# Kernel optimization log

Measured on AMD Instinct MI355X. Metric: run time of the kernel, lower is better.

## Reference

```python
import jax, jax.numpy as jnp
import numpy as np

N = 4096      # num_nodes
B = 32        # batch
U = 64        # num_units
L = 2         # num_rnn_layers
K = 2         # max_diffusion_step
OUT = 1       # output_dim (also decoder input_dim)
NM = 2 * K + 1  # num_matrices: 2 supports * K cheb steps + identity


def _random_walk_T(adj):
    # calculate_random_walk_matrix(adj).T : (D^-1 W)^T
    d = adj.sum(axis=1)
    return (adj / d[:, None]).T


def setup_inputs():
    key = jax.random.key(0)
    ks = jax.random.split(key, 16)
    adj = jax.random.uniform(ks[0], (N, N), dtype=jnp.float32)
    S_fwd = _random_walk_T(adj)      # forward transition, transposed
    S_bwd = _random_walk_T(adj.T)    # backward transition, transposed

    inputs = jax.random.normal(ks[1], (B, N, OUT), dtype=jnp.float32)
    hidden_state = jax.random.normal(ks[2], (L, B, N, U), dtype=jnp.float32) * 0.1

    D0 = OUT + U   # layer 0 gconv input width
    D1 = U + U     # layer 1 gconv input width
    s = 0.05
    Wg0 = jax.random.normal(ks[3], (NM * D0, 2 * U), jnp.float32) * s
    bg0 = jnp.ones((2 * U,), jnp.float32)          # bias_start = 1.0 for gates
    Wc0 = jax.random.normal(ks[4], (NM * D0, U), jnp.float32) * s
    bc0 = jnp.zeros((U,), jnp.float32)
    Wg1 = jax.random.normal(ks[5], (NM * D1, 2 * U), jnp.float32) * s
    bg1 = jnp.ones((2 * U,), jnp.float32)
    Wc1 = jax.random.normal(ks[6], (NM * D1, U), jnp.float32) * s
    bc1 = jnp.zeros((U,), jnp.float32)
    Wp = jax.random.normal(ks[7], (U, OUT), jnp.float32) * s
    bp = jnp.zeros((OUT,), jnp.float32)
    return {
        "inputs": inputs, "hidden_state": hidden_state,
        "S_fwd": S_fwd, "S_bwd": S_bwd,
        "Wg0": Wg0, "bg0": bg0, "Wc0": Wc0, "bc0": bc0,
        "Wg1": Wg1, "bg1": bg1, "Wc1": Wc1, "bc1": bc1,
        "Wp": Wp, "bp": bp,
    }


def _gconv(supports, x, h, W, b):
    # diffusion graph convolution with Chebyshev recursion (DCRNN)
    x0 = jnp.concatenate([x, h], axis=-1)      # (B, N, D)
    xs = [x0]
    for S in supports:
        x1 = jnp.einsum('mn,bnd->bmd', S, x0)
        xs.append(x1)
        xk_2, xk_1 = x0, x1
        for _ in range(K - 1):
            x2 = 2.0 * jnp.einsum('mn,bnd->bmd', S, xk_1) - xk_2
            xs.append(x2)
            xk_2, xk_1 = xk_1, x2
    X = jnp.concatenate(xs, axis=-1)           # (B, N, NM*D)
    return X @ W + b


def _dcgru_cell(supports, x, h, Wg, bg, Wc, bc):
    value = jax.nn.sigmoid(_gconv(supports, x, h, Wg, bg))   # (B, N, 2U)
    r, u = jnp.split(value, 2, axis=-1)
    c = jnp.tanh(_gconv(supports, x, r * h, Wc, bc))
    return u * h + (1.0 - u) * c


def reference(inputs, hidden_state, S_fwd, S_bwd,
              Wg0, bg0, Wc0, bc0, Wg1, bg1, Wc1, bc1, Wp, bp):
    supports = (S_fwd, S_bwd)
    layer_params = [(Wg0, bg0, Wc0, bc0), (Wg1, bg1, Wc1, bc1)]
    out = inputs
    new_hidden = []
    for i, (Wg, bg, Wc, bc) in enumerate(layer_params):
        h = _dcgru_cell(supports, out, hidden_state[i], Wg, bg, Wc, bc)
        new_hidden.append(h)
        out = h
    predict = out @ Wp + bp                    # (B, N, OUT)
    return predict, jnp.stack(new_hidden)
```

## Files before the change

### kernel.cpp

```cpp
#include <hip/hip_runtime.h>

typedef unsigned short u16;
typedef unsigned int u32;
typedef unsigned long long u64;
typedef short v8s __attribute__((ext_vector_type(8)));
typedef float v4f __attribute__((ext_vector_type(4)));

#define NN 4096
#define BATCH 32

__device__ __forceinline__ float b2f(u16 u) {
  union { u32 i; float f; } c; c.i = ((u32)u) << 16; return c.f;
}
__device__ __forceinline__ u16 f2b(float f) {
  union { float f; u32 i; } c; c.f = f;
  u32 x = c.i;
  return (u16)((x + 0x7fffu + ((x >> 16) & 1u)) >> 16);
}
__device__ __forceinline__ u32 pk2(float a, float b) {
  return (u32)f2b(a) | ((u32)f2b(b) << 16);
}

typedef const __attribute__((address_space(1))) u32* gp_t;
typedef __attribute__((address_space(3))) u32* lp_t;
__device__ __forceinline__ void gld16(const u16* g, u16* l) {
  __builtin_amdgcn_global_load_lds((gp_t)g, (lp_t)l, 16, 0, 0);
}

#define CBAR() asm volatile("" ::: "memory")
#define BARRIER() do { CBAR(); __builtin_amdgcn_s_barrier(); CBAR(); } while (0)
#define LGKM0() asm volatile("s_waitcnt lgkmcnt(0)" ::: "memory")
#define VMC4() asm volatile("s_waitcnt vmcnt(4)" ::: "memory")
#define VMC3() asm volatile("s_waitcnt vmcnt(3)" ::: "memory")
#define VMC0() asm volatile("s_waitcnt vmcnt(0)" ::: "memory")

__global__ __launch_bounds__(256) void cvtS(const float* __restrict__ S,
                                            u16* __restrict__ Sb) {
  const u64 idx = ((u64)blockIdx.x * 256 + threadIdx.x) * 8;
  const float4 a = *(const float4*)(S + idx);
  const float4 b = *(const float4*)(S + idx + 4);
  uint4 o;
  o.x = pk2(a.x, a.y); o.y = pk2(a.z, a.w);
  o.z = pk2(b.x, b.y); o.w = pk2(b.z, b.w);
  *(uint4*)(Sb + idx) = o;
}

__global__ __launch_bounds__(512, 2) void gemm256(const u16* __restrict__ A,
                                                  const u16* __restrict__ B,
                                                  u16* __restrict__ Ct,
                                                  const u16* __restrict__ Xt) {
  __shared__ __align__(16) u16 lds[65536];
  const int t = threadIdx.x;
  const int wave = t >> 6, lane = t & 63;
  const int q = lane >> 4, r16 = lane & 15;
  const int wm = wave >> 2, wn = wave & 3;

  const int nwg = (int)(gridDim.x * gridDim.y);
  const int bid = (int)(blockIdx.y * gridDim.x + blockIdx.x);
  const int swz = (bid & 7) * (nwg >> 3) + (bid >> 3);
  const int m0 = (swz & 15) << 8;
  const int c0 = (swz >> 4) << 8;

  v4f acc[8][4];
  const v4f vz = {0.f, 0.f, 0.f, 0.f};
#pragma unroll
  for (int i = 0; i < 8; ++i)
#pragma unroll
    for (int j = 0; j < 4; ++j) acc[i][j] = vz;

  const int srow = t >> 3;
  const int sslot = ((t & 7) ^ (srow & 7)) << 3;
  const u16* pA = A + (u64)(m0 + srow) * NN + sslot;
  const u16* pB = B + (u64)(c0 + srow) * NN + sslot;
  const u64 rstep = (u64)64 * NN;
  const u64 hstep = (u64)128 * NN;
  u16* lw = lds + (wave << 9);

  const int sw8 = (q ^ (r16 & 7)) << 3;
  const int aBase = (wm << 13) + (r16 << 6) + sw8;
  const int bBase = 16384 + ((wn >> 1) << 13) + ((wn & 1) << 12) + (r16 << 6) + sw8;

  const int NT = NN >> 6;

  gld16(pA, lw);
  gld16(pA + rstep, lw + 4096);
  gld16(pA + hstep, lw + 8192);
  gld16(pA + hstep + rstep, lw + 12288);
  gld16(pB, lw + 16384);
  gld16(pB + rstep, lw + 20480);
  gld16(pB + hstep, lw + 24576);
  gld16(pB + hstep + rstep, lw + 28672);
  gld16(pB + 64, lw + 32768 + 16384);
  gld16(pB + 64 + rstep, lw + 32768 + 20480);
  gld16(pB + 64 + hstep, lw + 32768 + 24576);
  gld16(pB + 64 + hstep + rstep, lw + 32768 + 28672);
  VMC4();
  BARRIER();

  v8s af[4][2], bf01[2][2], bf23[2][2];
#pragma unroll
  for (int i = 0; i < 4; ++i) {
    const int a = aBase + (i << 10);
    af[i][0] = *(const v8s*)(lds + a);
    af[i][1] = *(const v8s*)(lds + (a ^ 32));
  }
#pragma unroll
  for (int j = 0; j < 2; ++j) {
    const int b = bBase + (j << 10);
    bf01[j][0] = *(const v8s*)(lds + b);
    bf01[j][1] = *(const v8s*)(lds + (b ^ 32));
  }

#pragma unroll 2
  for (int T = 0; T < NT; ++T) {
    const int bo = (T & 1) << 15;
    const int no = bo ^ 32768;
    const u64 ka = (u64)(T + 1 < NT ? T + 1 : NT - 1) << 6;
    const u64 kb = (u64)(T + 2 < NT ? T + 2 : NT - 1) << 6;

    gld16(pA + ka, lw + no);
    gld16(pA + ka + rstep, lw + no + 4096);
#pragma unroll
    for (int j = 0; j < 2; ++j) {
      const int b = bo + bBase + ((2 + j) << 10);
      bf23[j][0] = *(const v8s*)(lds + b);
      bf23[j][1] = *(const v8s*)(lds + (b ^ 32));
    }
    __builtin_amdgcn_s_setprio(1);
#pragma unroll
    for (int i = 0; i < 4; ++i)
#pragma unroll
      for (int j = 0; j < 2; ++j) {
        acc[i][j] = __builtin_amdgcn_mfma_f32_16x16x32_bf16(af[i][0], bf01[j][0], acc[i][j], 0, 0, 0);
        acc[i][j] = __builtin_amdgcn_mfma_f32_16x16x32_bf16(af[i][1], bf01[j][1], acc[i][j], 0, 0, 0);
      }
    __builtin_amdgcn_s_setprio(0);

    gld16(pA + hstep + ka, lw + no + 8192);
    gld16(pA + hstep + ka + rstep, lw + no + 12288);
    LGKM0();
    BARRIER();
    __builtin_amdgcn_s_setprio(1);
#pragma unroll
    for (int i = 0; i < 4; ++i)
#pragma unroll
      for (int j = 0; j < 2; ++j) {
        acc[i][2 + j] = __builtin_amdgcn_mfma_f32_16x16x32_bf16(af[i][0], bf23[j][0], acc[i][2 + j], 0, 0, 0);
        acc[i][2 + j] = __builtin_amdgcn_mfma_f32_16x16x32_bf16(af[i][1], bf23[j][1], acc[i][2 + j], 0, 0, 0);
      }
    __builtin_amdgcn_s_setprio(0);
#pragma unroll
    for (int i = 0; i < 4; ++i) {
      const int a = bo + aBase + ((4 + i) << 10);
      af[i][0] = *(const v8s*)(lds + a);
      af[i][1] = *(const v8s*)(lds + (a ^ 32));
    }
    __builtin_amdgcn_sched_barrier(0);

    gld16(pB + kb, lw + bo + 16384);
    gld16(pB + kb + rstep, lw + bo + 20480);
    __builtin_amdgcn_s_setprio(1);
#pragma unroll
    for (int i = 0; i < 4; ++i)
#pragma unroll
      for (int j = 0; j < 2; ++j) {
        acc[4 + i][2 + j] = __builtin_amdgcn_mfma_f32_16x16x32_bf16(af[i][0], bf23[j][0], acc[4 + i][2 + j], 0, 0, 0);
        acc[4 + i][2 + j] = __builtin_amdgcn_mfma_f32_16x16x32_bf16(af[i][1], bf23[j][1], acc[4 + i][2 + j], 0, 0, 0);
      }
    __builtin_amdgcn_s_setprio(0);

    gld16(pB + hstep + kb, lw + bo + 24576);
    gld16(pB + hstep + kb + rstep, lw + bo + 28672);
    VMC4();
    BARRIER();
    __builtin_amdgcn_s_setprio(1);
#pragma unroll
    for (int i = 0; i < 4; ++i)
#pragma unroll
      for (int j = 0; j < 2; ++j) {
        acc[4 + i][j] = __builtin_amdgcn_mfma_f32_16x16x32_bf16(af[i][0], bf01[j][0], acc[4 + i][j], 0, 0, 0);
        acc[4 + i][j] = __builtin_amdgcn_mfma_f32_16x16x32_bf16(af[i][1], bf01[j][1], acc[4 + i][j], 0, 0, 0);
      }
    __builtin_amdgcn_s_setprio(0);
#pragma unroll
    for (int i = 0; i < 4; ++i) {
      const int a = no + aBase + (i << 10);
      af[i][0] = *(const v8s*)(lds + a);
      af[i][1] = *(const v8s*)(lds + (a ^ 32));
    }
#pragma unroll
    for (int j = 0; j < 2; ++j) {
      const int b = no + bBase + (j << 10);
      bf01[j][0] = *(const v8s*)(lds + b);
      bf01[j][1] = *(const v8s*)(lds + (b ^ 32));
    }
    __builtin_amdgcn_sched_barrier(0);
  }

  VMC0();
  __syncthreads();
#pragma unroll
  for (int i = 0; i < 8; ++i)
#pragma unroll
    for (int j = 0; j < 4; ++j) {
      const int cl = (wn << 6) + (j << 4) + r16;
      const int ml = (wm << 7) + (i << 4) + (q << 2);
      const int phys = (cl << 8) + ((((ml >> 3) ^ (cl & 7)) << 3) | (ml & 7));
      uint2 pv;
      pv.x = pk2(acc[i][j][0], acc[i][j][1]);
      pv.y = pk2(acc[i][j][2], acc[i][j][3]);
      *(uint2*)(lds + phys) = pv;
    }
  __syncthreads();
#pragma unroll
  for (int it = 0; it < 16; ++it) {
    const int f = (it << 9) + t;
    const int cl = f >> 5, sl = f & 31;
    const int phys = (cl << 8) + ((sl ^ (cl & 7)) << 3);
    union { uint4 v; u16 e[8]; } tv;
    tv.v = *(const uint4*)(lds + phys);
    const u64 gi = (u64)(c0 + cl) * NN + m0 + (sl << 3);
    if (Xt) {
      union { uint4 v; u16 e[8]; } xv, ov;
      xv.v = *(const uint4*)(Xt + gi);
#pragma unroll
      for (int s = 0; s < 8; ++s) ov.e[s] = f2b(2.f * b2f(tv.e[s]) - b2f(xv.e[s]));
      *(uint4*)(Ct + gi) = ov.v;
    } else {
      *(uint4*)(Ct + gi) = tv.v;
    }
  }
}

__global__ __launch_bounds__(512, 2) void gemm192(const u16* __restrict__ A,
                                                  const u16* __restrict__ B,
                                                  u16* __restrict__ Ct,
                                                  const u16* __restrict__ Xt) {
  __shared__ __align__(16) u16 lds[57344];
  const int t = threadIdx.x;
  const int wave = t >> 6, lane = t & 63;
  const int q = lane >> 4, r16 = lane & 15;
  const int wm = wave >> 2, wn = wave & 3;

  const int nwg = (int)(gridDim.x * gridDim.y);
  const int bid = (int)(blockIdx.y * gridDim.x + blockIdx.x);
  const int swz = (bid & 7) * (nwg >> 3) + (bid >> 3);
  const int m0 = (swz & 15) << 8;
  const int c0 = (swz >> 4) * 192;

  v4f acc[8][3];
  const v4f vz = {0.f, 0.f, 0.f, 0.f};
#pragma unroll
  for (int i = 0; i < 8; ++i)
#pragma unroll
    for (int j = 0; j < 3; ++j) acc[i][j] = vz;

  const int srow = t >> 3;
  const int sslot = ((t & 7) ^ (srow & 7)) << 3;
  const u16* pA = A + (u64)(m0 + srow) * NN + sslot;
  const u16* pB = B + (u64)(c0 + srow) * NN + sslot;
  const u64 rstep = (u64)64 * NN;
  u16* lw = lds + (wave << 9);

  const int sw8 = (q ^ (r16 & 7)) << 3;
  const int aBase = (wm << 13) + (r16 << 6) + sw8;
  const int bBase = 16384 + wn * 3072 + (r16 << 6) + sw8;

  const int NT = NN >> 6;

  gld16(pA, lw);
  gld16(pA + rstep, lw + 4096);
  gld16(pA + 2 * rstep, lw + 8192);
  gld16(pA + 3 * rstep, lw + 12288);
  gld16(pB, lw + 16384);
  gld16(pB + rstep, lw + 20480);
  gld16(pB + 2 * rstep, lw + 24576);
  gld16(pB + 64, lw + 28672 + 16384);
  gld16(pB + 64 + rstep, lw + 28672 + 20480);
  gld16(pB + 64 + 2 * rstep, lw + 28672 + 24576);
  VMC3();
  BARRIER();

  v8s af[4][2], bf01[2][2], bf2[2];
#pragma unroll
  for (int i = 0; i < 4; ++i) {
    const int a = aBase + (i << 10);
    af[i][0] = *(const v8s*)(lds + a);
    af[i][1] = *(const v8s*)(lds + (a ^ 32));
  }
#pragma unroll
  for (int j = 0; j < 2; ++j) {
    const int b = bBase + (j << 10);
    bf01[j][0] = *(const v8s*)(lds + b);
    bf01[j][1] = *(const v8s*)(lds + (b ^ 32));
  }

#pragma unroll 2
  for (int T = 0; T < NT; ++T) {
    const int bo = (T & 1) ? 28672 : 0;
    const int no = bo ^ 28672;
    const u64 ka = (u64)(T + 1 < NT ? T + 1 : NT - 1) << 6;
    const u64 kb = (u64)(T + 2 < NT ? T + 2 : NT - 1) << 6;

    gld16(pA + ka, lw + no);
    gld16(pA + ka + rstep, lw + no + 4096);
    {
      const int b = bo + bBase + 2048;
      bf2[0] = *(const v8s*)(lds + b);
      bf2[1] = *(const v8s*)(lds + (b ^ 32));
    }
    __builtin_amdgcn_s_setprio(1);
#pragma unroll
    for (int i = 0; i < 4; ++i)
#pragma unroll
      for (int j = 0; j < 2; ++j) {
        acc[i][j] = __builtin_amdgcn_mfma_f32_16x16x32_bf16(af[i][0], bf01[j][0], acc[i][j], 0, 0, 0);
        acc[i][j] = __builtin_amdgcn_mfma_f32_16x16x32_bf16(af[i][1], bf01[j][1], acc[i][j], 0, 0, 0);
      }
    __builtin_amdgcn_s_setprio(0);

    gld16(pA + ka + 2 * rstep, lw + no + 8192);
    gld16(pA + ka + 3 * rstep, lw + no + 12288);
    LGKM0();
    BARRIER();
    __builtin_amdgcn_s_setprio(1);
#pragma unroll
    for (int i = 0; i < 4; ++i) {
      acc[i][2] = __builtin_amdgcn_mfma_f32_16x16x32_bf16(af[i][0], bf2[0], acc[i][2], 0, 0, 0);
      acc[i][2] = __builtin_amdgcn_mfma_f32_16x16x32_bf16(af[i][1], bf2[1], acc[i][2], 0, 0, 0);
    }
    __builtin_amdgcn_s_setprio(0);
#pragma unroll
    for (int i = 0; i < 4; ++i) {
      const int a = bo + aBase + ((4 + i) << 10);
      af[i][0] = *(const v8s*)(lds + a);
      af[i][1] = *(const v8s*)(lds + (a ^ 32));
    }
    __builtin_amdgcn_sched_barrier(0);

    gld16(pB + kb, lw + bo + 16384);
    gld16(pB + kb + rstep, lw + bo + 20480);
    __builtin_amdgcn_s_setprio(1);
#pragma unroll
    for (int i = 0; i < 4; ++i) {
      acc[4 + i][2] = __builtin_amdgcn_mfma_f32_16x16x32_bf16(af[i][0], bf2[0], acc[4 + i][2], 0, 0, 0);
      acc[4 + i][2] = __builtin_amdgcn_mfma_f32_16x16x32_bf16(af[i][1], bf2[1], acc[4 + i][2], 0, 0, 0);
    }
    __builtin_amdgcn_s_setprio(0);

    gld16(pB + kb + 2 * rstep, lw + bo + 24576);
    __builtin_amdgcn_s_setprio(1);
#pragma unroll
    for (int i = 0; i < 4; ++i)
#pragma unroll
      for (int j = 0; j < 2; ++j) {
        acc[4 + i][j] = __builtin_amdgcn_mfma_f32_16x16x32_bf16(af[i][0], bf01[j][0], acc[4 + i][j], 0, 0, 0);
        acc[4 + i][j] = __builtin_amdgcn_mfma_f32_16x16x32_bf16(af[i][1], bf01[j][1], acc[4 + i][j], 0, 0, 0);
      }
    __builtin_amdgcn_s_setprio(0);
    VMC3();
    BARRIER();
#pragma unroll
    for (int i = 0; i < 4; ++i) {
      const int a = no + aBase + (i << 10);
      af[i][0] = *(const v8s*)(lds + a);
      af[i][1] = *(const v8s*)(lds + (a ^ 32));
    }
#pragma unroll
    for (int j = 0; j < 2; ++j) {
      const int b = no + bBase + (j << 10);
      bf01[j][0] = *(const v8s*)(lds + b);
      bf01[j][1] = *(const v8s*)(lds + (b ^ 32));
    }
    __builtin_amdgcn_sched_barrier(0);
  }

  VMC0();
  __syncthreads();
#pragma unroll
  for (int i = 0; i < 8; ++i)
#pragma unroll
    for (int j = 0; j < 3; ++j) {
      const int cl = wn * 48 + j * 16 + r16;
      const int ml = (wm << 7) + (i << 4) + (q << 2);
      const int phys = (cl << 8) + ((((ml >> 3) ^ (cl & 7)) << 3) | (ml & 7));
      uint2 pv;
      pv.x = pk2(acc[i][j][0], acc[i][j][1]);
      pv.y = pk2(acc[i][j][2], acc[i][j][3]);
      *(uint2*)(lds + phys) = pv;
    }
  __syncthreads();
#pragma unroll
  for (int it = 0; it < 12; ++it) {
    const int f = (it << 9) + t;
    const int cl = f >> 5, sl = f & 31;
    const int phys = (cl << 8) + ((sl ^ (cl & 7)) << 3);
    union { uint4 v; u16 e[8]; } tv;
    tv.v = *(const uint4*)(lds + phys);
    const u64 gi = (u64)(c0 + cl) * NN + m0 + (sl << 3);
    if (Xt) {
      union { uint4 v; u16 e[8]; } xv, ov;
      xv.v = *(const uint4*)(Xt + gi);
#pragma unroll
      for (int s = 0; s < 8; ++s) ov.e[s] = f2b(2.f * b2f(tv.e[s]) - b2f(xv.e[s]));
      *(uint4*)(Ct + gi) = ov.v;
    } else {
      *(uint4*)(Ct + gi) = tv.v;
    }
  }
}

__global__ __launch_bounds__(256) void gemm_s(const float* __restrict__ A,
                                              const u16* __restrict__ B,
                                              u16* __restrict__ Ct,
                                              const u16* __restrict__ Xt) {
  __shared__ __align__(16) u16 As[4096];
  __shared__ __align__(16) u16 Bs[4096];
  __shared__ __align__(16) u16 T[16384];
  const int t = threadIdx.x;
  const int wave = t >> 6, lane = t & 63;
  const int m0 = blockIdx.x << 7, c0 = blockIdx.y << 7;
  const int wm = (wave >> 1) << 6, wc = (wave & 1) << 6;
  const int q = lane >> 4, r16 = lane & 15;
  v4f acc[4][4];
  const v4f vz = {0.f, 0.f, 0.f, 0.f};
#pragma unroll
  for (int i = 0; i < 4; ++i)
#pragma unroll
    for (int j = 0; j < 4; ++j) acc[i][j] = vz;

  const int sr = t >> 2;
  const int sc = (t & 3) << 3;
  const u64 abase = (u64)(m0 + sr) * NN + sc;
  const u64 bbase = (u64)(c0 + sr) * NN + sc;
  const u64 rstep = (u64)64 * NN;
  u16* as0 = As + sr * 32 + sc;
  u16* as1 = As + (64 + sr) * 32 + sc;
  u16* bs0 = Bs + sr * 32 + sc;
  u16* bs1 = Bs + (64 + sr) * 32 + sc;

  for (int k0 = 0; k0 < NN; k0 += 32) {
    const float4 a0l = *(const float4*)(A + abase + k0);
    const float4 a0h = *(const float4*)(A + abase + k0 + 4);
    const float4 a1l = *(const float4*)(A + abase + rstep + k0);
    const float4 a1h = *(const float4*)(A + abase + rstep + k0 + 4);
    const uint4 b0 = *(const uint4*)(B + bbase + k0);
    const uint4 b1 = *(const uint4*)(B + bbase + rstep + k0);
    uint4 pa0, pa1;
    pa0.x = pk2(a0l.x, a0l.y); pa0.y = pk2(a0l.z, a0l.w);
    pa0.z = pk2(a0h.x, a0h.y); pa0.w = pk2(a0h.z, a0h.w);
    pa1.x = pk2(a1l.x, a1l.y); pa1.y = pk2(a1l.z, a1l.w);
    pa1.z = pk2(a1h.x, a1h.y); pa1.w = pk2(a1h.z, a1h.w);
    __syncthreads();
    *(uint4*)as0 = pa0;
    *(uint4*)as1 = pa1;
    *(uint4*)bs0 = b0;
    *(uint4*)bs1 = b1;
    __syncthreads();
    v8s af[4], bf[4];
#pragma unroll
    for (int i = 0; i < 4; ++i)
      af[i] = *(const v8s*)(As + ((wm + i * 16 + r16) << 5) + (q << 3));
#pragma unroll
    for (int j = 0; j < 4; ++j)
      bf[j] = *(const v8s*)(Bs + ((wc + j * 16 + r16) << 5) + (q << 3));
#pragma unroll
    for (int i = 0; i < 4; ++i)
#pragma unroll
      for (int j = 0; j < 4; ++j)
        acc[i][j] = __builtin_amdgcn_mfma_f32_16x16x32_bf16(af[i], bf[j], acc[i][j], 0, 0, 0);
  }
#pragma unroll
  for (int i = 0; i < 4; ++i)
#pragma unroll
    for (int j = 0; j < 4; ++j) {
      const int cl = wc + j * 16 + r16;
      const int mm = wm + i * 16 + (q << 2);
      uint2 pv;
      pv.x = pk2(acc[i][j][0], acc[i][j][1]);
      pv.y = pk2(acc[i][j][2], acc[i][j][3]);
      *(uint2*)(T + (cl << 7) + mm) = pv;
    }
  __syncthreads();
#pragma unroll
  for (int it = 0; it < 8; ++it) {
    const int flat = it * 256 + t;
    const int cl = flat >> 4;
    const int seg = (flat & 15) << 3;
    const u64 gi = (u64)(c0 + cl) * NN + m0 + seg;
    union { uint4 v; u16 e[8]; } tv;
    tv.v = *(uint4*)(T + (cl << 7) + seg);
    if (Xt) {
      union { uint4 v; u16 e[8]; } xv, ov;
      xv.v = *(const uint4*)(Xt + gi);
#pragma unroll
      for (int s = 0; s < 8; ++s) ov.e[s] = f2b(2.f * b2f(tv.e[s]) - b2f(xv.e[s]));
      *(uint4*)(Ct + gi) = ov.v;
    } else {
      *(uint4*)(Ct + gi) = tv.v;
    }
  }
}

template <int DP, int KTOT>
__global__ __launch_bounds__(256) void proj_k(const u16* __restrict__ Wt,
                                              const u16* __restrict__ F,
                                              const float* __restrict__ bias,
                                              u16* __restrict__ outp,
                                              const int JSTR, const int ACT) {
  __shared__ __align__(16) u16 As2[2048];
  __shared__ __align__(16) u16 Bs2[4096];
  const int t = threadIdx.x;
  const int wave = t >> 6, lane = t & 63;
  const int q = lane >> 4, r16 = lane & 15;
  const int n0 = blockIdx.x << 7;
  const int j0 = blockIdx.y << 6;
  const int b = blockIdx.z;
  v4f acc[4][2];
  const v4f vz = {0.f, 0.f, 0.f, 0.f};
#pragma unroll
  for (int i = 0; i < 4; ++i) { acc[i][0] = vz; acc[i][1] = vz; }

  const int ar = t >> 2, ac = (t & 3) << 3;
  const u64 wbase = (u64)(j0 + ar) * KTOT + ac;

  for (int k0 = 0; k0 < KTOT; k0 += 32) {
    const uint4 av = *(const uint4*)(Wt + wbase + k0);
    uint4 bv[2];
#pragma unroll
    for (int ci = 0; ci < 2; ++ci) {
      const int c = ci * 256 + t;
      const int kr = c >> 4;
      const int seg = (c & 15) << 3;
      const int kk = k0 + kr;
      const int i = kk / DP;
      const int d = kk - i * DP;
      bv[ci] = *(const uint4*)(F + ((u64)i * (BATCH * DP) + (u64)b * DP + d) * NN + n0 + seg);
    }
    __syncthreads();
    *(uint4*)(As2 + ar * 32 + ac) = av;
#pragma unroll
    for (int ci = 0; ci < 2; ++ci) {
      const int c = ci * 256 + t;
      const int kr = c >> 4;
      const int seg = (c & 15) << 3;
      *(uint4*)(Bs2 + (kr << 7) + seg) = bv[ci];
    }
    __syncthreads();
    v8s af[4], bf[2];
#pragma unroll
    for (int i = 0; i < 4; ++i)
      af[i] = *(const v8s*)(As2 + ((i * 16 + r16) << 5) + (q << 3));
#pragma unroll
    for (int jj = 0; jj < 2; ++jj) {
      const int nn = (wave << 5) + jj * 16 + r16;
      v8s v;
#pragma unroll
      for (int s = 0; s < 8; ++s) v[s] = (short)Bs2[(((q << 3) + s) << 7) + nn];
      bf[jj] = v;
    }
#pragma unroll
    for (int i = 0; i < 4; ++i)
#pragma unroll
      for (int jj = 0; jj < 2; ++jj)
        acc[i][jj] = __builtin_amdgcn_mfma_f32_16x16x32_bf16(af[i], bf[jj], acc[i][jj], 0, 0, 0);
  }
#pragma unroll
  for (int i = 0; i < 4; ++i)
#pragma unroll
    for (int jj = 0; jj < 2; ++jj)
#pragma unroll
      for (int r = 0; r < 4; ++r) {
        const int j = j0 + i * 16 + (q << 2) + r;
        const int n = n0 + (wave << 5) + jj * 16 + r16;
        float v = acc[i][jj][r] + bias[j];
        v = ACT ? (1.f - 2.f / (__expf(2.f * v) + 1.f)) : (1.f / (1.f + __expf(-v)));
        outp[((u64)b * JSTR + j) * NN + n] = f2b(v);
      }
}

__global__ __launch_bounds__(256) void repackW(const float* __restrict__ W, u16* __restrict__ Wt,
                                               const int D, const int DP, const int KTOT,
                                               const int J) {
  const int idx = blockIdx.x * 256 + threadIdx.x;
  if (idx >= J * KTOT) return;
  const int j = idx / KTOT, k = idx - j * KTOT;
  const int i = k / DP, d = k - i * DP;
  u16 v = 0;
  if (i < 5 && d < D) v = f2b(W[(i * D + d) * J + j]);
  Wt[idx] = v;
}

__global__ __launch_bounds__(256) void pack0(const float* __restrict__ x,
                                             const float* __restrict__ hid0,
                                             u16* __restrict__ F0) {
  __shared__ __align__(16) u16 Hs[64 * 72];
  const int b = blockIdx.y, n0 = blockIdx.x << 6, t = threadIdx.x;
  const int r = t >> 2, ds = t & 3;
  const float* hrow = hid0 + ((u64)b * NN + n0 + r) * 64;
#pragma unroll
  for (int c4 = 0; c4 < 4; ++c4) {
    const float4 v = *(const float4*)(hrow + ds * 16 + c4 * 4);
    uint2 p;
    p.x = pk2(v.x, v.y);
    p.y = pk2(v.z, v.w);
    *(uint2*)(Hs + r * 72 + ds * 16 + c4 * 4) = p;
  }
  __syncthreads();
#pragma unroll
  for (int c2 = 0; c2 < 2; ++c2) {
    union { uint4 v; u16 h[8]; } o;
#pragma unroll
    for (int s = 0; s < 8; ++s) o.h[s] = Hs[(ds * 16 + c2 * 8 + s) * 72 + r];
    *(uint4*)(F0 + ((u64)b * 72 + 1 + r) * NN + n0 + ds * 16 + c2 * 8) = o.v;
  }
  if (t < 64) {
    F0[(u64)b * 72 * NN + n0 + t] = f2b(x[(u64)b * NN + n0 + t]);
  } else if (t < 120) {
    const int tt = t - 64;
    const int row = 65 + (tt >> 3), seg = (tt & 7) << 3;
    uint4 z; z.x = z.y = z.z = z.w = 0;
    *(uint4*)(F0 + ((u64)b * 72 + row) * NN + n0 + seg) = z;
  }
}

__global__ __launch_bounds__(256) void pack1(const float* __restrict__ hid1,
                                             u16* __restrict__ F1) {
  __shared__ __align__(16) u16 Hs[64 * 72];
  const int b = blockIdx.y, n0 = blockIdx.x << 6, t = threadIdx.x;
  const int r = t >> 2, ds = t & 3;
  const float* hrow = hid1 + ((u64)b * NN + n0 + r) * 64;
#pragma unroll
  for (int c4 = 0; c4 < 4; ++c4) {
    const float4 v = *(const float4*)(hrow + ds * 16 + c4 * 4);
    uint2 p;
    p.x = pk2(v.x, v.y);
    p.y = pk2(v.z, v.w);
    *(uint2*)(Hs + r * 72 + ds * 16 + c4 * 4) = p;
  }
  __syncthreads();
#pragma unroll
  for (int c2 = 0; c2 < 2; ++c2) {
    union { uint4 v; u16 h[8]; } o;
#pragma unroll
    for (int s = 0; s < 8; ++s) o.h[s] = Hs[(ds * 16 + c2 * 8 + s) * 72 + r];
    *(uint4*)(F1 + ((u64)b * 128 + 64 + r) * NN + n0 + ds * 16 + c2 * 8) = o.v;
  }
}

__global__ __launch_bounds__(256) void candpack(const u16* __restrict__ G, u16* __restrict__ F,
                                                const int DP, const int OFF) {
  const int u = blockIdx.x * 256 + threadIdx.x;
  const int b = u >> 15;
  const int d = (u >> 9) & 63;
  const int seg = (u & 511) << 3;
  union { uint4 v; u16 h[8]; } g, f, o;
  g.v = *(const uint4*)(G + ((u64)b * 128 + d) * NN + seg);
  u16* fp = F + ((u64)b * DP + OFF + d) * NN + seg;
  f.v = *(const uint4*)fp;
#pragma unroll
  for (int s = 0; s < 8; ++s) o.h[s] = f2b(b2f(f.h[s]) * b2f(g.h[s]));
  *(uint4*)fp = o.v;
}

__global__ __launch_bounds__(256) void hnew_k(const u16* __restrict__ G,
                                              const float* __restrict__ hidL,
                                              u16* __restrict__ HnF,
                                              float* __restrict__ outH) {
  __shared__ __align__(16) float Hs[64 * 72];
  __shared__ __align__(16) float T2[64 * 72];
  const int b = blockIdx.y, n0 = blockIdx.x << 6, t = threadIdx.x;
  const int r = t >> 2, ds = t & 3;
  const float* hrow = hidL + ((u64)b * NN + n0 + r) * 64;
#pragma unroll
  for (int c4 = 0; c4 < 4; ++c4)
    *(float4*)(Hs + r * 72 + ds * 16 + c4 * 4) = *(const float4*)(hrow + ds * 16 + c4 * 4);
  __syncthreads();
#pragma unroll
  for (int c2 = 0; c2 < 2; ++c2) {
    const int ncol = ds * 16 + c2 * 8;
    union { uint4 v; u16 h[8]; } uv, cv, o;
    uv.v = *(const uint4*)(G + ((u64)b * 128 + 64 + r) * NN + n0 + ncol);
    cv.v = *(const uint4*)(G + ((u64)b * 128 + r) * NN + n0 + ncol);
#pragma unroll
    for (int s = 0; s < 8; ++s) {
      const int nl = ncol + s;
      const float uu = b2f(uv.h[s]);
      const float hh = Hs[nl * 72 + r];
      const float cc = b2f(cv.h[s]);
      const float v = uu * hh + (1.f - uu) * cc;
      o.h[s] = f2b(v);
      T2[nl * 72 + r] = v;
    }
    *(uint4*)(HnF + ((u64)b * 128 + r) * NN + n0 + ncol) = o.v;
  }
  __syncthreads();
  const int nl2 = t >> 2, dseg = (t & 3) << 4;
#pragma unroll
  for (int c4 = 0; c4 < 4; ++c4) {
    const float4 v = *(const float4*)(T2 + nl2 * 72 + dseg + c4 * 4);
    *(float4*)(outH + ((u64)b * NN + n0 + nl2) * 64 + dseg + c4 * 4) = v;
  }
}

__global__ __launch_bounds__(256) void predictk(const float* __restrict__ H1bnd,
                                                const float* __restrict__ Wp,
                                                const float* __restrict__ bp,
                                                float* __restrict__ outp) {
  __shared__ float w[64];
  __shared__ float bb;
  const int t = threadIdx.x;
  if (t < 64) w[t] = Wp[t];
  if (t == 64) bb = bp[0];
  __syncthreads();
  const int idx = blockIdx.x * 256 + t;
  const float* h = H1bnd + (u64)idx * 64;
  float acc = bb;
#pragma unroll
  for (int c4 = 0; c4 < 16; ++c4) {
    const float4 v = *(const float4*)(h + c4 * 4);
    acc += v.x * w[c4 * 4] + v.y * w[c4 * 4 + 1] + v.z * w[c4 * 4 + 2] + v.w * w[c4 * 4 + 3];
  }
  outp[idx] = acc;
}

extern "C" void kernel_launch(void* const* d_in, const int* in_sizes, int n_in,
                              void* d_out, int out_size, void* d_ws, size_t ws_size,
                              hipStream_t stream) {
  const float* X   = (const float*)d_in[0];
  const float* HID = (const float*)d_in[1];
  const float* Sf  = (const float*)d_in[2];
  const float* Sb  = (const float*)d_in[3];
  const float* Wg0 = (const float*)d_in[4];
  const float* bg0 = (const float*)d_in[5];
  const float* Wc0 = (const float*)d_in[6];
  const float* bc0 = (const float*)d_in[7];
  const float* Wg1 = (const float*)d_in[8];
  const float* bg1 = (const float*)d_in[9];
  const float* Wc1 = (const float*)d_in[10];
  const float* bc1 = (const float*)d_in[11];
  const float* Wp  = (const float*)d_in[12];
  const float* bp  = (const float*)d_in[13];
  float* OUT = (float*)d_out;
  char* ws = (char*)d_ws;

  u16* F = (u16*)(ws);
  u16* G = (u16*)(ws + 167772160ull);
  const u64 NEED_BIG = 167772160ull + 33554432ull + 2ull * 33554432ull + 393216ull;
  const bool big = ws_size >= NEED_BIG;
  u16* Sfb = (u16*)(ws + 167772160ull + 33554432ull);
  u16* Sbb = Sfb + (u64)NN * NN;
  u16* WT = big ? (Sbb + (u64)NN * NN)
                : (u16*)(ws + 167772160ull + 33554432ull);
  u16* Wg0t = WT;
  u16* Wc0t = Wg0t + 128 * 384;
  u16* Wg1t = Wc0t + 64 * 384;
  u16* Wc1t = Wg1t + 128 * 640;

  const float* HID1 = HID + (u64)32 * 4096 * 64;
  float* OUT_H0 = OUT + 131072;
  float* OUT_H1 = OUT + 131072 + 8388608;

  hipMemsetAsync(ws + (u64)11520 * NN * 2, 0, (u64)2304 * NN * 2, stream);

  if (big) {
    cvtS<<<8192, 256, 0, stream>>>(Sf, Sfb);
    cvtS<<<8192, 256, 0, stream>>>(Sb, Sbb);
  }

  repackW<<<(128 * 384 + 255) / 256, 256, 0, stream>>>(Wg0, Wg0t, 65, 72, 384, 128);
  repackW<<<(64 * 384 + 255) / 256, 256, 0, stream>>>(Wc0, Wc0t, 65, 72, 384, 64);
  repackW<<<(128 * 640 + 255) / 256, 256, 0, stream>>>(Wg1, Wg1t, 128, 128, 640, 128);
  repackW<<<(64 * 640 + 255) / 256, 256, 0, stream>>>(Wc1, Wc1t, 128, 128, 640, 64);

  pack0<<<dim3(64, 32), 256, 0, stream>>>(X, HID, F);
  const u64 R0 = (u64)2304 * NN;
  const dim3 g192(16, 12);
  if (big) {
    gemm192<<<g192, 512, 0, stream>>>(Sfb, F, F + R0, nullptr);
    gemm192<<<g192, 512, 0, stream>>>(Sbb, F, F + 3 * R0, nullptr);
    gemm192<<<g192, 512, 0, stream>>>(Sfb, F + R0, F + 2 * R0, F);
    gemm192<<<g192, 512, 0, stream>>>(Sbb, F + 3 * R0, F + 4 * R0, F);
  } else {
    gemm_s<<<dim3(32, 18), 256, 0, stream>>>(Sf, F, F + R0, nullptr);
    gemm_s<<<dim3(32, 18), 256, 0, stream>>>(Sb, F, F + 3 * R0, nullptr);
    gemm_s<<<dim3(32, 18), 256, 0, stream>>>(Sf, F + R0, F + 2 * R0, F);
    gemm_s<<<dim3(32, 18), 256, 0, stream>>>(Sb, F + 3 * R0, F + 4 * R0, F);
  }
  proj_k<72, 384><<<dim3(32, 2, 32), 256, 0, stream>>>(Wg0t, F, bg0, G, 128, 0);
  candpack<<<4096, 256, 0, stream>>>(G, F, 72, 1);
  if (big) {
    gemm192<<<g192, 512, 0, stream>>>(Sfb, F, F + R0, nullptr);
    gemm192<<<g192, 512, 0, stream>>>(Sbb, F, F + 3 * R0, nullptr);
    gemm192<<<g192, 512, 0, stream>>>(Sfb, F + R0, F + 2 * R0, F);
    gemm192<<<g192, 512, 0, stream>>>(Sbb, F + 3 * R0, F + 4 * R0, F);
  } else {
    gemm_s<<<dim3(32, 18), 256, 0, stream>>>(Sf, F, F + R0, nullptr);
    gemm_s<<<dim3(32, 18), 256, 0, stream>>>(Sb, F, F + 3 * R0, nullptr);
    gemm_s<<<dim3(32, 18), 256, 0, stream>>>(Sf, F + R0, F + 2 * R0, F);
    gemm_s<<<dim3(32, 18), 256, 0, stream>>>(Sb, F + 3 * R0, F + 4 * R0, F);
  }
  proj_k<72, 384><<<dim3(32, 1, 32), 256, 0, stream>>>(Wc0t, F, bc0, G, 128, 1);
  hnew_k<<<dim3(64, 32), 256, 0, stream>>>(G, HID, F, OUT_H0);

  pack1<<<dim3(64, 32), 256, 0, stream>>>(HID1, F);
  const u64 R1 = (u64)4096 * NN;
  const dim3 g256(16, 16);
  if (big) {
    gemm256<<<g256, 512, 0, stream>>>(Sfb, F, F + R1, nullptr);
    gemm256<<<g256, 512, 0, stream>>>(Sbb, F, F + 3 * R1, nullptr);
    gemm256<<<g256, 512, 0, stream>>>(Sfb, F + R1, F + 2 * R1, F);
    gemm256<<<g256, 512, 0, stream>>>(Sbb, F + 3 * R1, F + 4 * R1, F);
  } else {
    gemm_s<<<dim3(32, 32), 256, 0, stream>>>(Sf, F, F + R1, nullptr);
    gemm_s<<<dim3(32, 32), 256, 0, stream>>>(Sb, F, F + 3 * R1, nullptr);
    gemm_s<<<dim3(32, 32), 256, 0, stream>>>(Sf, F + R1, F + 2 * R1, F);
    gemm_s<<<dim3(32, 32), 256, 0, stream>>>(Sb, F + 3 * R1, F + 4 * R1, F);
  }
  proj_k<128, 640><<<dim3(32, 2, 32), 256, 0, stream>>>(Wg1t, F, bg1, G, 128, 0);
  candpack<<<4096, 256, 0, stream>>>(G, F, 128, 64);
  if (big) {
    gemm256<<<g256, 512, 0, stream>>>(Sfb, F, F + R1, nullptr);
    gemm256<<<g256, 512, 0, stream>>>(Sbb, F, F + 3 * R1, nullptr);
    gemm256<<<g256, 512, 0, stream>>>(Sfb, F + R1, F + 2 * R1, F);
    gemm256<<<g256, 512, 0, stream>>>(Sbb, F + 3 * R1, F + 4 * R1, F);
  } else {
    gemm_s<<<dim3(32, 32), 256, 0, stream>>>(Sf, F, F + R1, nullptr);
    gemm_s<<<dim3(32, 32), 256, 0, stream>>>(Sb, F, F + 3 * R1, nullptr);
    gemm_s<<<dim3(32, 32), 256, 0, stream>>>(Sf, F + R1, F + 2 * R1, F);
    gemm_s<<<dim3(32, 32), 256, 0, stream>>>(Sb, F + 3 * R1, F + 4 * R1, F);
  }
  proj_k<128, 640><<<dim3(32, 1, 32), 256, 0, stream>>>(Wc1t, F, bc1, G, 128, 1);
  hnew_k<<<dim3(64, 32), 256, 0, stream>>>(G, HID1, F, OUT_H1);

  predictk<<<512, 256, 0, stream>>>(OUT_H1, Wp, bp, OUT);
}
```

Before: 1.875 ms.

## Retile layer-0 diffusion GEMM to 144 columns and fuse elementwise epilogues

The layer-0 support GEMM now uses a 256x144 tile with all eight waves split along M (2x9 accumulators per wave) instead of 256x192 with a 2x4 wave grid. The grid becomes 16x16 to cover the 2304 columns, which spreads the work over more workgroups. Separately, the r*h candidate packing is fused into the gate projection epilogue, and the output projection is fused into the final hnew kernel, removing two launches and a pass over memory. The risks are lower per-wave reuse in the narrower GEMM and a read-modify-write of F inside proj_k.

```diff
diff --git a/kernel.cpp b/kernel.cpp
--- a/kernel.cpp
+++ b/kernel.cpp
@@ -170,7 +170,7 @@
     __builtin_amdgcn_s_setprio(0);
 
     gld16(pB + hstep + kb, lw + bo + 24576);
-    gld16(pB + hstep + kb + rstep, lw + bo + 28672);
+    gld16(pB + hstep + rstep + kb, lw + bo + 28672);
     VMC4();
     BARRIER();
     __builtin_amdgcn_s_setprio(1);
@@ -232,7 +232,7 @@
   }
 }
 
-__global__ __launch_bounds__(512, 2) void gemm192(const u16* __restrict__ A,
+__global__ __launch_bounds__(512, 2) void gemm144(const u16* __restrict__ A,
                                                   const u16* __restrict__ B,
                                                   u16* __restrict__ Ct,
                                                   const u16* __restrict__ Xt) {
@@ -240,20 +240,20 @@
   const int t = threadIdx.x;
   const int wave = t >> 6, lane = t & 63;
   const int q = lane >> 4, r16 = lane & 15;
-  const int wm = wave >> 2, wn = wave & 3;
+  const int wm = wave;
 
   const int nwg = (int)(gridDim.x * gridDim.y);
   const int bid = (int)(blockIdx.y * gridDim.x + blockIdx.x);
   const int swz = (bid & 7) * (nwg >> 3) + (bid >> 3);
   const int m0 = (swz & 15) << 8;
-  const int c0 = (swz >> 4) * 192;
-
-  v4f acc[8][3];
+  const int c0 = (swz >> 4) * 144;
+
+  v4f acc[2][9];
   const v4f vz = {0.f, 0.f, 0.f, 0.f};
 #pragma unroll
-  for (int i = 0; i < 8; ++i)
-#pragma unroll
-    for (int j = 0; j < 3; ++j) acc[i][j] = vz;
+  for (int i = 0; i < 2; ++i)
+#pragma unroll
+    for (int j = 0; j < 9; ++j) acc[i][j] = vz;
 
   const int srow = t >> 3;
   const int sslot = ((t & 7) ^ (srow & 7)) << 3;
@@ -263,8 +263,8 @@
   u16* lw = lds + (wave << 9);
 
   const int sw8 = (q ^ (r16 & 7)) << 3;
-  const int aBase = (wm << 13) + (r16 << 6) + sw8;
-  const int bBase = 16384 + wn * 3072 + (r16 << 6) + sw8;
+  const int aBase = (wm << 11) + (r16 << 6) + sw8;
+  const int bBase = 16384 + (r16 << 6) + sw8;
 
   const int NT = NN >> 6;
 
@@ -281,18 +281,18 @@
   VMC3();
   BARRIER();
 
-  v8s af[4][2], bf01[2][2], bf2[2];
-#pragma unroll
-  for (int i = 0; i < 4; ++i) {
+  v8s af[2][2], bfA[5][2], bfB[4][2];
+#pragma unroll
+  for (int i = 0; i < 2; ++i) {
     const int a = aBase + (i << 10);
     af[i][0] = *(const v8s*)(lds + a);
     af[i][1] = *(const v8s*)(lds + (a ^ 32));
   }
 #pragma unroll
-  for (int j = 0; j < 2; ++j) {
+  for (int j = 0; j < 5; ++j) {
     const int b = bBase + (j << 10);
-    bf01[j][0] = *(const v8s*)(lds + b);
-    bf01[j][1] = *(const v8s*)(lds + (b ^ 32));
+    bfA[j][0] = *(const v8s*)(lds + b);
+    bfA[j][1] = *(const v8s*)(lds + (b ^ 32));
   }
 
 #pragma unroll 2
@@ -304,19 +304,18 @@
 
     gld16(pA + ka, lw + no);
     gld16(pA + ka + rstep, lw + no + 4096);
-    {
-      const int b = bo + bBase + 2048;
-      bf2[0] = *(const v8s*)(lds + b);
-      bf2[1] = *(const v8s*)(lds + (b ^ 32));
+#pragma unroll
+    for (int j = 0; j < 4; ++j) {
+      const int b = bo + bBase + ((5 + j) << 10);
+      bfB[j][0] = *(const v8s*)(lds + b);
+      bfB[j][1] = *(const v8s*)(lds + (b ^ 32));
     }
     __builtin_amdgcn_s_setprio(1);
 #pragma unroll
-    for (int i = 0; i < 4; ++i)
-#pragma unroll
-      for (int j = 0; j < 2; ++j) {
-        acc[i][j] = __builtin_amdgcn_mfma_f32_16x16x32_bf16(af[i][0], bf01[j][0], acc[i][j], 0, 0, 0);
-        acc[i][j] = __builtin_amdgcn_mfma_f32_16x16x32_bf16(af[i][1], bf01[j][1], acc[i][j], 0, 0, 0);
-      }
+    for (int i = 0; i < 2; ++i)
+#pragma unroll
+      for (int j = 0; j < 5; ++j)
+        acc[i][j] = __builtin_amdgcn_mfma_f32_16x16x32_bf16(af[i][0], bfA[j][0], acc[i][j], 0, 0, 0);
     __builtin_amdgcn_s_setprio(0);
 
     gld16(pA + ka + 2 * rstep, lw + no + 8192);
@@ -325,52 +324,43 @@
     BARRIER();
     __builtin_amdgcn_s_setprio(1);
 #pragma unroll
-    for (int i = 0; i < 4; ++i) {
-      acc[i][2] = __builtin_amdgcn_mfma_f32_16x16x32_bf16(af[i][0], bf2[0], acc[i][2], 0, 0, 0);
-      acc[i][2] = __builtin_amdgcn_mfma_f32_16x16x32_bf16(af[i][1], bf2[1], acc[i][2], 0, 0, 0);
-    }
+    for (int i = 0; i < 2; ++i)
+#pragma unroll
+      for (int j = 0; j < 5; ++j)
+        acc[i][j] = __builtin_amdgcn_mfma_f32_16x16x32_bf16(af[i][1], bfA[j][1], acc[i][j], 0, 0, 0);
     __builtin_amdgcn_s_setprio(0);
-#pragma unroll
-    for (int i = 0; i < 4; ++i) {
-      const int a = bo + aBase + ((4 + i) << 10);
-      af[i][0] = *(const v8s*)(lds + a);
-      af[i][1] = *(const v8s*)(lds + (a ^ 32));
-    }
-    __builtin_amdgcn_sched_barrier(0);
 
     gld16(pB + kb, lw + bo + 16384);
     gld16(pB + kb + rstep, lw + bo + 20480);
     __builtin_amdgcn_s_setprio(1);
 #pragma unroll
-    for (int i = 0; i < 4; ++i) {
-      acc[4 + i][2] = __builtin_amdgcn_mfma_f32_16x16x32_bf16(af[i][0], bf2[0], acc[4 + i][2], 0, 0, 0);
-      acc[4 + i][2] = __builtin_amdgcn_mfma_f32_16x16x32_bf16(af[i][1], bf2[1], acc[4 + i][2], 0, 0, 0);
-    }
+    for (int i = 0; i < 2; ++i)
+#pragma unroll
+      for (int j = 0; j < 4; ++j)
+        acc[i][5 + j] = __builtin_amdgcn_mfma_f32_16x16x32_bf16(af[i][0], bfB[j][0], acc[i][5 + j], 0, 0, 0);
     __builtin_amdgcn_s_setprio(0);
 
     gld16(pB + kb + 2 * rstep, lw + bo + 24576);
     __builtin_amdgcn_s_setprio(1);
 #pragma unroll
-    for (int i = 0; i < 4; ++i)
-#pragma unroll
-      for (int j = 0; j < 2; ++j) {
-        acc[4 + i][j] = __builtin_amdgcn_mfma_f32_16x16x32_bf16(af[i][0], bf01[j][0], acc[4 + i][j], 0, 0, 0);
-        acc[4 + i][j] = __builtin_amdgcn_mfma_f32_16x16x32_bf16(af[i][1], bf01[j][1], acc[4 + i][j], 0, 0, 0);
-      }
+    for (int i = 0; i < 2; ++i)
+#pragma unroll
+      for (int j = 0; j < 4; ++j)
+        acc[i][5 + j] = __builtin_amdgcn_mfma_f32_16x16x32_bf16(af[i][1], bfB[j][1], acc[i][5 + j], 0, 0, 0);
     __builtin_amdgcn_s_setprio(0);
     VMC3();
     BARRIER();
 #pragma unroll
-    for (int i = 0; i < 4; ++i) {
+    for (int i = 0; i < 2; ++i) {
       const int a = no + aBase + (i << 10);
       af[i][0] = *(const v8s*)(lds + a);
       af[i][1] = *(const v8s*)(lds + (a ^ 32));
     }
 #pragma unroll
-    for (int j = 0; j < 2; ++j) {
+    for (int j = 0; j < 5; ++j) {
       const int b = no + bBase + (j << 10);
-      bf01[j][0] = *(const v8s*)(lds + b);
-      bf01[j][1] = *(const v8s*)(lds + (b ^ 32));
+      bfA[j][0] = *(const v8s*)(lds + b);
+      bfA[j][1] = *(const v8s*)(lds + (b ^ 32));
     }
     __builtin_amdgcn_sched_barrier(0);
   }
@@ -378,11 +368,11 @@
   VMC0();
   __syncthreads();
 #pragma unroll
-  for (int i = 0; i < 8; ++i)
-#pragma unroll
-    for (int j = 0; j < 3; ++j) {
-      const int cl = wn * 48 + j * 16 + r16;
-      const int ml = (wm << 7) + (i << 4) + (q << 2);
+  for (int i = 0; i < 2; ++i)
+#pragma unroll
+    for (int j = 0; j < 9; ++j) {
+      const int cl = j * 16 + r16;
+      const int ml = (wm << 5) + (i << 4) + (q << 2);
       const int phys = (cl << 8) + ((((ml >> 3) ^ (cl & 7)) << 3) | (ml & 7));
       uint2 pv;
       pv.x = pk2(acc[i][j][0], acc[i][j][1]);
@@ -391,7 +381,7 @@
     }
   __syncthreads();
 #pragma unroll
-  for (int it = 0; it < 12; ++it) {
+  for (int it = 0; it < 9; ++it) {
     const int f = (it << 9) + t;
     const int cl = f >> 5, sl = f & 31;
     const int phys = (cl << 8) + ((sl ^ (cl & 7)) << 3);
@@ -507,7 +497,9 @@
                                               const u16* __restrict__ F,
                                               const float* __restrict__ bias,
                                               u16* __restrict__ outp,
-                                              const int JSTR, const int ACT) {
+                                              const int JSTR, const int ACT,
+                                              u16* __restrict__ Fmul,
+                                              const int OFF) {
   __shared__ __align__(16) u16 As2[2048];
   __shared__ __align__(16) u16 Bs2[4096];
   const int t = threadIdx.x;
@@ -575,7 +567,12 @@
         const int n = n0 + (wave << 5) + jj * 16 + r16;
         float v = acc[i][jj][r] + bias[j];
         v = ACT ? (1.f - 2.f / (__expf(2.f * v) + 1.f)) : (1.f / (1.f + __expf(-v)));
-        outp[((u64)b * JSTR + j) * NN + n] = f2b(v);
+        if (Fmul && j < 64) {
+          u16* fp = Fmul + ((u64)b * DP + OFF + j) * NN + n;
+          *fp = f2b(b2f(*fp) * v);
+        } else {
+          outp[((u64)b * JSTR + j) * NN + n] = f2b(v);
+        }
       }
 }
 
@@ -648,30 +645,24 @@
   }
 }
 
-__global__ __launch_bounds__(256) void candpack(const u16* __restrict__ G, u16* __restrict__ F,
-                                                const int DP, const int OFF) {
-  const int u = blockIdx.x * 256 + threadIdx.x;
-  const int b = u >> 15;
-  const int d = (u >> 9) & 63;
-  const int seg = (u & 511) << 3;
-  union { uint4 v; u16 h[8]; } g, f, o;
-  g.v = *(const uint4*)(G + ((u64)b * 128 + d) * NN + seg);
-  u16* fp = F + ((u64)b * DP + OFF + d) * NN + seg;
-  f.v = *(const uint4*)fp;
-#pragma unroll
-  for (int s = 0; s < 8; ++s) o.h[s] = f2b(b2f(f.h[s]) * b2f(g.h[s]));
-  *(uint4*)fp = o.v;
-}
-
 __global__ __launch_bounds__(256) void hnew_k(const u16* __restrict__ G,
                                               const float* __restrict__ hidL,
                                               u16* __restrict__ HnF,
-                                              float* __restrict__ outH) {
+                                              float* __restrict__ outH,
+                                              const float* __restrict__ Wp,
+                                              const float* __restrict__ bp,
+                                              float* __restrict__ outPred) {
   __shared__ __align__(16) float Hs[64 * 72];
   __shared__ __align__(16) float T2[64 * 72];
+  __shared__ float wsh[64];
+  __shared__ float bbs;
   const int b = blockIdx.y, n0 = blockIdx.x << 6, t = threadIdx.x;
   const int r = t >> 2, ds = t & 3;
   const float* hrow = hidL + ((u64)b * NN + n0 + r) * 64;
+  if (outPred) {
+    if (t < 64) wsh[t] = Wp[t];
+    if (t == 64) bbs = bp[0];
+  }
 #pragma unroll
   for (int c4 = 0; c4 < 4; ++c4)
     *(float4*)(Hs + r * 72 + ds * 16 + c4 * 4) = *(const float4*)(hrow + ds * 16 + c4 * 4);
@@ -701,27 +692,12 @@
     const float4 v = *(const float4*)(T2 + nl2 * 72 + dseg + c4 * 4);
     *(float4*)(outH + ((u64)b * NN + n0 + nl2) * 64 + dseg + c4 * 4) = v;
   }
-}
-
-__global__ __launch_bounds__(256) void predictk(const float* __restrict__ H1bnd,
-                                                const float* __restrict__ Wp,
-                                                const float* __restrict__ bp,
-                                                float* __restrict__ outp) {
-  __shared__ float w[64];
-  __shared__ float bb;
-  const int t = threadIdx.x;
-  if (t < 64) w[t] = Wp[t];
-  if (t == 64) bb = bp[0];
-  __syncthreads();
-  const int idx = blockIdx.x * 256 + t;
-  const float* h = H1bnd + (u64)idx * 64;
-  float acc = bb;
-#pragma unroll
-  for (int c4 = 0; c4 < 16; ++c4) {
-    const float4 v = *(const float4*)(h + c4 * 4);
-    acc += v.x * w[c4 * 4] + v.y * w[c4 * 4 + 1] + v.z * w[c4 * 4 + 2] + v.w * w[c4 * 4 + 3];
-  }
-  outp[idx] = acc;
+  if (outPred && t < 64) {
+    float s = bbs;
+#pragma unroll
+    for (int rr = 0; rr < 64; ++rr) s += T2[t * 72 + rr] * wsh[rr];
+    outPred[(u64)b * NN + n0 + t] = s;
+  }
 }
 
 extern "C" void kernel_launch(void* const* d_in, const int* in_sizes, int n_in,
@@ -775,33 +751,32 @@
 
   pack0<<<dim3(64, 32), 256, 0, stream>>>(X, HID, F);
   const u64 R0 = (u64)2304 * NN;
-  const dim3 g192(16, 12);
+  const dim3 g144(16, 16);
   if (big) {
-    gemm192<<<g192, 512, 0, stream>>>(Sfb, F, F + R0, nullptr);
-    gemm192<<<g192, 512, 0, stream>>>(Sbb, F, F + 3 * R0, nullptr);
-    gemm192<<<g192, 512, 0, stream>>>(Sfb, F + R0, F + 2 * R0, F);
-    gemm192<<<g192, 512, 0, stream>>>(Sbb, F + 3 * R0, F + 4 * R0, F);
+    gemm144<<<g144, 512, 0, stream>>>(Sfb, F, F + R0, nullptr);
+    gemm144<<<g144, 512, 0, stream>>>(Sbb, F, F + 3 * R0, nullptr);
+    gemm144<<<g144, 512, 0, stream>>>(Sfb, F + R0, F + 2 * R0, F);
+    gemm144<<<g144, 512, 0, stream>>>(Sbb, F + 3 * R0, F + 4 * R0, F);
   } else {
     gemm_s<<<dim3(32, 18), 256, 0, stream>>>(Sf, F, F + R0, nullptr);
     gemm_s<<<dim3(32, 18), 256, 0, stream>>>(Sb, F, F + 3 * R0, nullptr);
     gemm_s<<<dim3(32, 18), 256, 0, stream>>>(Sf, F + R0, F + 2 * R0, F);
     gemm_s<<<dim3(32, 18), 256, 0, stream>>>(Sb, F + 3 * R0, F + 4 * R0, F);
   }
-  proj_k<72, 384><<<dim3(32, 2, 32), 256, 0, stream>>>(Wg0t, F, bg0, G, 128, 0);
-  candpack<<<4096, 256, 0, stream>>>(G, F, 72, 1);
+  proj_k<72, 384><<<dim3(32, 2, 32), 256, 0, stream>>>(Wg0t, F, bg0, G, 128, 0, F, 1);
   if (big) {
-    gemm192<<<g192, 512, 0, stream>>>(Sfb, F, F + R0, nullptr);
-    gemm192<<<g192, 512, 0, stream>>>(Sbb, F, F + 3 * R0, nullptr);
-    gemm192<<<g192, 512, 0, stream>>>(Sfb, F + R0, F + 2 * R0, F);
-    gemm192<<<g192, 512, 0, stream>>>(Sbb, F + 3 * R0, F + 4 * R0, F);
+    gemm144<<<g144, 512, 0, stream>>>(Sfb, F, F + R0, nullptr);
+    gemm144<<<g144, 512, 0, stream>>>(Sbb, F, F + 3 * R0, nullptr);
+    gemm144<<<g144, 512, 0, stream>>>(Sfb, F + R0, F + 2 * R0, F);
+    gemm144<<<g144, 512, 0, stream>>>(Sbb, F + 3 * R0, F + 4 * R0, F);
   } else {
     gemm_s<<<dim3(32, 18), 256, 0, stream>>>(Sf, F, F + R0, nullptr);
     gemm_s<<<dim3(32, 18), 256, 0, stream>>>(Sb, F, F + 3 * R0, nullptr);
     gemm_s<<<dim3(32, 18), 256, 0, stream>>>(Sf, F + R0, F + 2 * R0, F);
     gemm_s<<<dim3(32, 18), 256, 0, stream>>>(Sb, F + 3 * R0, F + 4 * R0, F);
   }
-  proj_k<72, 384><<<dim3(32, 1, 32), 256, 0, stream>>>(Wc0t, F, bc0, G, 128, 1);
-  hnew_k<<<dim3(64, 32), 256, 0, stream>>>(G, HID, F, OUT_H0);
+  proj_k<72, 384><<<dim3(32, 1, 32), 256, 0, stream>>>(Wc0t, F, bc0, G, 128, 1, nullptr, 0);
+  hnew_k<<<dim3(64, 32), 256, 0, stream>>>(G, HID, F, OUT_H0, nullptr, nullptr, nullptr);
 
   pack1<<<dim3(64, 32), 256, 0, stream>>>(HID1, F);
   const u64 R1 = (u64)4096 * NN;
@@ -817,8 +792,7 @@
     gemm_s<<<dim3(32, 32), 256, 0, stream>>>(Sf, F + R1, F + 2 * R1, F);
     gemm_s<<<dim3(32, 32), 256, 0, stream>>>(Sb, F + 3 * R1, F + 4 * R1, F);
   }
-  proj_k<128, 640><<<dim3(32, 2, 32), 256, 0, stream>>>(Wg1t, F, bg1, G, 128, 0);
-  candpack<<<4096, 256, 0, stream>>>(G, F, 128, 64);
+  proj_k<128, 640><<<dim3(32, 2, 32), 256, 0, stream>>>(Wg1t, F, bg1, G, 128, 0, F, 64);
   if (big) {
     gemm256<<<g256, 512, 0, stream>>>(Sfb, F, F + R1, nullptr);
     gemm256<<<g256, 512, 0, stream>>>(Sbb, F, F + 3 * R1, nullptr);
@@ -830,8 +804,6 @@
     gemm_s<<<dim3(32, 32), 256, 0, stream>>>(Sf, F + R1, F + 2 * R1, F);
     gemm_s<<<dim3(32, 32), 256, 0, stream>>>(Sb, F + 3 * R1, F + 4 * R1, F);
   }
-  proj_k<128, 640><<<dim3(32, 1, 32), 256, 0, stream>>>(Wc1t, F, bc1, G, 128, 1);
-  hnew_k<<<dim3(64, 32), 256, 0, stream>>>(G, HID1, F, OUT_H1);
-
-  predictk<<<512, 256, 0, stream>>>(OUT_H1, Wp, bp, OUT);
-}
+  proj_k<128, 640><<<dim3(32, 1, 32), 256, 0, stream>>>(Wc1t, F, bc1, G, 128, 1, nullptr, 0);
+  hnew_k<<<dim3(64, 32), 256, 0, stream>>>(G, HID1, F, OUT_H1, Wp, bp, OUT);
+}
```

Measured after the change: 1.935 ms. 3.2% more time.
